# Performance work log

Hardware: AMD Instinct MI355X
Metric: run time of the kernel (lower is better)

Reference implementation:

```python
import jax, jax.numpy as jnp
import numpy as np

NUM_HEADS = 8


def setup_inputs() -> dict:
    key = jax.random.key(0)
    ks = jax.random.split(key, 6)
    B, S, H = 2, 4096, 512
    Q = jax.random.normal(ks[0], (B, S, H), dtype=jnp.float32)
    K = jax.random.normal(ks[1], (B, S, H), dtype=jnp.float32)
    V = jax.random.normal(ks[2], (B, S, H), dtype=jnp.float32)
    risk_sigma = jax.random.uniform(ks[3], (B, 1), dtype=jnp.float32) * 0.2
    risk_lambda = jnp.array([2.0], dtype=jnp.float32)
    W_out = jax.random.normal(ks[4], (H, H), dtype=jnp.float32) * (1.0 / np.sqrt(H))
    b_out = jnp.zeros((H,), dtype=jnp.float32)
    return {"Q": Q, "K": K, "V": V, "risk_sigma": risk_sigma,
            "risk_lambda": risk_lambda, "W_out": W_out, "b_out": b_out}


def reference(Q, K, V, risk_sigma, risk_lambda, W_out, b_out):
    B, S, H = Q.shape
    nh = NUM_HEADS
    hd = H // nh
    # split heads: [B, S, nh, hd]
    q = Q.reshape(B, S, nh, hd)
    k = K.reshape(B, S, nh, hd)
    v = V.reshape(B, S, nh, hd)
    scale = 1.0 / jnp.sqrt(jnp.asarray(hd, dtype=Q.dtype))
    # [B, nh, S, S]
    scores = jnp.einsum('bshd,bthd->bhst', q, k) * scale
    # distance-based risk penalty
    pos = jnp.arange(S, dtype=Q.dtype)
    norm_dist = jnp.abs(pos[None, :] - pos[:, None]) / S  # [S, S]
    dist_sq = norm_dist ** 2
    sigma_c = jnp.clip(risk_sigma, 0.001, 0.2)            # [B, 1]
    sigma_n = (sigma_c - 0.001) / (0.2 - 0.001)
    lam = (risk_lambda / 10.0).reshape(())                 # scalar
    risk_term = lam * sigma_n[:, :, None, None] * dist_sq[None, None]  # [B,1,S,S]
    attn = jax.nn.softmax(scores - risk_term, axis=-1)
    ctx = jnp.einsum('bhst,bthd->bshd', attn, v).reshape(B, S, H)
    return ctx @ W_out.T + b_out
```

## Files before the change

kernel.cpp:

```cpp
#include <hip/hip_runtime.h>
#include <hip/hip_bf16.h>


#define S_LEN 4096
#define NHEAD 8
#define HD 64
#define HTOT 512

typedef __attribute__((ext_vector_type(8))) short short8;
typedef __attribute__((ext_vector_type(4))) float floatx4;
typedef __attribute__((ext_vector_type(8))) _Float16 half8;

#if __has_builtin(__builtin_amdgcn_exp2f)
#define EXP2F(x) __builtin_amdgcn_exp2f(x)
#else
#define EXP2F(x) exp2f(x)
#endif

__device__ __forceinline__ unsigned pack_bf16(float a, float b) {
    unsigned ua = __builtin_bit_cast(unsigned, a) + 0x8000u;
    unsigned ub = __builtin_bit_cast(unsigned, b) + 0x8000u;
    return __builtin_amdgcn_perm(ub, ua, 0x07060302u);
}

__device__ __forceinline__ unsigned short f2bf(float x) {
    unsigned u = __builtin_bit_cast(unsigned, x) + 0x8000u;
    return (unsigned short)(u >> 16);
}

__device__ __forceinline__ void async16(const unsigned short* g, unsigned short* l) {
    __builtin_amdgcn_global_load_lds(
        (const __attribute__((address_space(1))) unsigned int*)g,
        (__attribute__((address_space(3))) unsigned int*)l, 16, 0, 0);
}

__global__ __launch_bounds__(256) void prep_kernel(
    const float* __restrict__ K, unsigned short* __restrict__ K16,
    const float* __restrict__ V, unsigned short* __restrict__ Vt)
{
    const int tid = threadIdx.x;
    if (blockIdx.x < 2048) {
        size_t i = ((size_t)blockIdx.x * 256 + tid) * 8;
        float4 a = *(const float4*)(K + i);
        float4 b = *(const float4*)(K + i + 4);
        unsigned o[4] = {pack_bf16(a.x, a.y), pack_bf16(a.z, a.w),
                         pack_bf16(b.x, b.y), pack_bf16(b.z, b.w)};
        *(short8*)(K16 + i) = *(short8*)o;
    } else {
        __shared__ unsigned short T[64 * 66];
        const int blk = blockIdx.x - 2048;
        const int st = blk & 63;
        const int bh = blk >> 6;
        const int b = bh >> 3, h = bh & 7;
        const float* src = V + ((size_t)b * S_LEN + st * 64) * HTOT + h * HD;
        for (int i = 0; i < 4; i++) {
            int idx = tid + i * 256;
            int s = idx >> 4, c4 = idx & 15;
            float4 v = *(const float4*)(src + (size_t)s * HTOT + c4 * 4);
            T[(c4 * 4 + 0) * 66 + s] = f2bf(v.x);
            T[(c4 * 4 + 1) * 66 + s] = f2bf(v.y);
            T[(c4 * 4 + 2) * 66 + s] = f2bf(v.z);
            T[(c4 * 4 + 3) * 66 + s] = f2bf(v.w);
        }
        __syncthreads();
        unsigned short* dst = Vt + ((size_t)bh * 64) * S_LEN + st * 64;
        for (int i = 0; i < 2; i++) {
            int idx = tid + i * 256;
            int d = idx >> 3, c8 = idx & 7;
            uint2 lo = *(const uint2*)&T[d * 66 + c8 * 8];
            uint2 hi = *(const uint2*)&T[d * 66 + c8 * 8 + 4];
            unsigned o[4] = {lo.x, lo.y, hi.x, hi.y};
            *(short8*)(dst + (size_t)d * S_LEN + c8 * 8) = *(short8*)o;
        }
    }
}

__global__ __launch_bounds__(256) void attn_kernel(
    const float* __restrict__ Q, const unsigned short* __restrict__ K16,
    const unsigned short* __restrict__ Vt,
    const float* __restrict__ risk_sigma, const float* __restrict__ risk_lambda,
    _Float16* __restrict__ Cpart, float* __restrict__ Lpart)
{
    __shared__ unsigned short QPsh[128 * 72];
    __shared__ unsigned short Ksh[2][64 * 64];
    __shared__ unsigned short Vsh[2][64 * 64];

    const int tid  = threadIdx.x;
    const int wave = tid >> 6;
    const int lane = tid & 63;
    const int quad = lane >> 4;
    const int ln   = lane & 15;
    const int sw   = ln & 7;

    const int bid = blockIdx.x;
    const int ks  = bid & 1;
    const int qt  = (bid >> 1) & 31;
    const int h   = (bid >> 6) & 7;
    const int b   = bid >> 9;
    const int qbase = qt * 128;

    float sig = risk_sigma[b];
    sig = fminf(fmaxf(sig, 0.001f), 0.2f);
    const float sn   = (sig - 0.001f) * (1.0f / 0.199f);
    const float coef = risk_lambda[0] * 0.1f * sn;
    const float nc2 = -coef * (1.0f / 4096.0f) * (1.0f / 4096.0f) * 1.4426950408889634f;
    const float qscale = 0.125f * 1.4426950408889634f;

    const float* Qb = Q + (size_t)b * S_LEN * HTOT + (size_t)h * HD;
    const unsigned short* Kb = K16 + (size_t)b * S_LEN * HTOT + (size_t)h * HD;
    const unsigned short* Vb = Vt + ((size_t)(b * 8 + h) * 64) * S_LEN;

    const int rl  = lane >> 3;
    const int c8g = ((lane & 7) ^ rl) << 3;
    auto dma = [&](int buf, int kbase) {
        const unsigned short* gk = Kb + (size_t)(kbase + wave * 8 + rl) * HTOT + c8g;
        const unsigned short* gv = Vb + (size_t)(wave * 8 + rl) * S_LEN + kbase + c8g;
        async16(gk,              &Ksh[buf][wave * 512 + lane * 8]);
        async16(gk + 32 * HTOT,  &Ksh[buf][(wave + 4) * 512 + lane * 8]);
        async16(gv,              &Vsh[buf][wave * 512 + lane * 8]);
        async16(gv + 32 * S_LEN, &Vsh[buf][(wave + 4) * 512 + lane * 8]);
    };

    dma(0, ks * 2048);
    for (int i = 0; i < 8; i++) {
        int idx = tid + i * 256;
        int r = idx >> 4, c4 = idx & 15;
        float4 v = *(const float4*)(Qb + (size_t)(qbase + r) * HTOT + c4 * 4);
        uint2 o;
        o.x = pack_bf16(v.x * qscale, v.y * qscale);
        o.y = pack_bf16(v.z * qscale, v.w * qscale);
        *(uint2*)&QPsh[r * 72 + c4 * 4] = o;
    }
    __syncthreads();

    short8 qf[2][2];
    for (int nt = 0; nt < 2; nt++) {
        qf[nt][0] = *(const short8*)&QPsh[(wave * 32 + nt * 16 + ln) * 72 + quad * 8];
        qf[nt][1] = *(const short8*)&QPsh[(wave * 32 + nt * 16 + ln) * 72 + 32 + quad * 8];
    }
    unsigned short* Pw = &QPsh[wave * 32 * 72];

    const short sone = (short)0x3F80;
    const short8 ones = {sone, sone, sone, sone, sone, sone, sone, sone};

    floatx4 Oacc[2][4], Lacc[2];
    for (int nt = 0; nt < 2; nt++) {
        Lacc[nt] = (floatx4){0.f, 0.f, 0.f, 0.f};
        for (int dt = 0; dt < 4; dt++) Oacc[nt][dt] = (floatx4){0.f, 0.f, 0.f, 0.f};
    }

    const int qa = qbase + wave * 32;

    for (int kt = 0; kt < 32; ++kt) {
        const int kbase = ks * 2048 + kt * 64;
        const int cur = kt & 1;
        if (kt < 31) dma(1 - cur, kbase + 64);
        const unsigned short* Kc = Ksh[cur];
        const unsigned short* Vc = Vsh[cur];

        const float dq = (float)(qa + ln - kbase);
        for (int jt = 0; jt < 4; jt++) {
            const int krow = (jt * 16 + ln) * 64;
            short8 ak0 = *(const short8*)&Kc[krow + ((quad ^ sw) << 3)];
            short8 ak1 = *(const short8*)&Kc[krow + (((quad + 4) ^ sw) << 3)];
            #pragma unroll
            for (int nt = 0; nt < 2; nt++) {
                floatx4 s = (floatx4){0.f, 0.f, 0.f, 0.f};
                s = __builtin_amdgcn_mfma_f32_16x16x32_bf16(ak0, qf[nt][0], s, 0, 0, 0);
                s = __builtin_amdgcn_mfma_f32_16x16x32_bf16(ak1, qf[nt][1], s, 0, 0, 0);
                float d = dq + (float)(nt * 16 - jt * 16 - quad * 4);
                float p[4];
                #pragma unroll
                for (int r = 0; r < 4; r++) {
                    float arg = __builtin_fmaf(nc2, d * d, s[r]);
                    p[r] = EXP2F(arg);
                    d -= 1.0f;
                }
                uint2 o;
                o.x = pack_bf16(p[0], p[1]);
                o.y = pack_bf16(p[2], p[3]);
                *(uint2*)&Pw[(nt * 16 + ln) * 72 + jt * 16 + quad * 4] = o;
            }
        }
        asm volatile("s_waitcnt lgkmcnt(0)" ::: "memory");
        __builtin_amdgcn_wave_barrier();

        short8 pf[2][2];
        for (int nt = 0; nt < 2; nt++) {
            pf[nt][0] = *(const short8*)&Pw[(nt * 16 + ln) * 72 + quad * 8];
            pf[nt][1] = *(const short8*)&Pw[(nt * 16 + ln) * 72 + 32 + quad * 8];
        }
        for (int dt = 0; dt < 4; dt++) {
            const int vrow = (dt * 16 + ln) * 64;
            short8 bv0 = *(const short8*)&Vc[vrow + ((quad ^ sw) << 3)];
            short8 bv1 = *(const short8*)&Vc[vrow + (((quad + 4) ^ sw) << 3)];
            #pragma unroll
            for (int nt = 0; nt < 2; nt++) {
                Oacc[nt][dt] = __builtin_amdgcn_mfma_f32_16x16x32_bf16(pf[nt][0], bv0, Oacc[nt][dt], 0, 0, 0);
                Oacc[nt][dt] = __builtin_amdgcn_mfma_f32_16x16x32_bf16(pf[nt][1], bv1, Oacc[nt][dt], 0, 0, 0);
            }
        }
        #pragma unroll
        for (int nt = 0; nt < 2; nt++) {
            Lacc[nt] = __builtin_amdgcn_mfma_f32_16x16x32_bf16(pf[nt][0], ones, Lacc[nt], 0, 0, 0);
            Lacc[nt] = __builtin_amdgcn_mfma_f32_16x16x32_bf16(pf[nt][1], ones, Lacc[nt], 0, 0, 0);
        }
        __syncthreads();
    }

    _Float16* Cw = Cpart + (size_t)bid * (128 * 64);
    for (int nt = 0; nt < 2; nt++) {
        if (ln == 0) {
            #pragma unroll
            for (int r = 0; r < 4; r++)
                Lpart[bid * 128 + wave * 32 + nt * 16 + quad * 4 + r] = Lacc[nt][r];
        }
        float rl4[4];
        #pragma unroll
        for (int r = 0; r < 4; r++) rl4[r] = 1.0f / Lacc[nt][r];
        for (int dt = 0; dt < 4; dt++)
            #pragma unroll
            for (int r = 0; r < 4; r++) {
                int q = wave * 32 + nt * 16 + quad * 4 + r;
                Cw[q * 64 + dt * 16 + ln] = (_Float16)(Oacc[nt][dt][r] * rl4[r]);
            }
    }
}

__global__ __launch_bounds__(256) void projc_kernel(
    const _Float16* __restrict__ Cpart, const float* __restrict__ Lpart,
    const float* __restrict__ W, const float* __restrict__ bias,
    float* __restrict__ out)
{
    __shared__ unsigned short Ash[64 * 40];
    __shared__ unsigned short Bsh[128 * 40];
    __shared__ float2 Lw[8][64];

    const int tid = threadIdx.x;
    const int wave = tid >> 6, lane = tid & 63, quad = lane >> 4, ln = lane & 15;
    const int wr = wave >> 1, wc = wave & 1;
    const int m0 = blockIdx.y * 64;
    const int nb = blockIdx.x * 128;
    const int b = m0 >> 12, qt = (m0 >> 7) & 31, qoff = m0 & 127;

    for (int i = 0; i < 2; i++) {
        int e = tid + i * 256;
        int hh = e >> 6, r = e & 63;
        int tile = (b * 8 + hh) * 32 + qt;
        float l0 = Lpart[(size_t)(tile * 2 + 0) * 128 + qoff + r];
        float l1 = Lpart[(size_t)(tile * 2 + 1) * 128 + qoff + r];
        float inv = 1.0f / (l0 + l1);
        Lw[hh][r] = (float2){l0 * inv, l1 * inv};
    }

    floatx4 acc[2][4];
    for (int i = 0; i < 2; i++)
        for (int j = 0; j < 4; j++) acc[i][j] = (floatx4){0.f, 0.f, 0.f, 0.f};

    const int ar = tid >> 2, ac8 = tid & 3;

    for (int kt = 0; kt < 16; ++kt) {
        const int k0 = kt * 32;
        const int h = k0 >> 6, d0 = k0 & 63;
        __syncthreads();
        {
            int tile = (b * 8 + h) * 32 + qt;
            const _Float16* C0 = Cpart + (size_t)(tile * 2) * (128 * 64)
                                 + (size_t)(qoff + ar) * 64 + d0 + ac8 * 8;
            const _Float16* C1 = C0 + 128 * 64;
            half8 a0 = *(const half8*)C0;
            half8 a1 = *(const half8*)C1;
            float2 w = Lw[h][ar];
            unsigned o[4];
            #pragma unroll
            for (int k = 0; k < 4; k++) {
                float v0 = w.x * (float)a0[2 * k]     + w.y * (float)a1[2 * k];
                float v1 = w.x * (float)a0[2 * k + 1] + w.y * (float)a1[2 * k + 1];
                o[k] = pack_bf16(v0, v1);
            }
            *(short8*)&Ash[ar * 40 + ac8 * 8] = *(short8*)o;
        }
        for (int i = 0; i < 4; i++) {
            int idx = tid + i * 256;
            int r = idx >> 3, c4 = idx & 7;
            float4 v = *(const float4*)&W[(size_t)(nb + r) * 512 + k0 + c4 * 4];
            uint2 o;
            o.x = pack_bf16(v.x, v.y);
            o.y = pack_bf16(v.z, v.w);
            *(uint2*)&Bsh[r * 40 + c4 * 4] = o;
        }
        __syncthreads();
        short8 af[2], bf[4];
        for (int i = 0; i < 2; i++)
            af[i] = *(const short8*)&Ash[(wr * 32 + i * 16 + ln) * 40 + quad * 8];
        for (int j = 0; j < 4; j++)
            bf[j] = *(const short8*)&Bsh[(wc * 64 + j * 16 + ln) * 40 + quad * 8];
        for (int i = 0; i < 2; i++)
            for (int j = 0; j < 4; j++)
                acc[i][j] = __builtin_amdgcn_mfma_f32_16x16x32_bf16(af[i], bf[j], acc[i][j], 0, 0, 0);
    }

    for (int i = 0; i < 2; i++) {
        int row = m0 + wr * 32 + i * 16 + quad * 4;
        for (int j = 0; j < 4; j++) {
            int col = nb + wc * 64 + j * 16 + ln;
            float bv = bias[col];
            #pragma unroll
            for (int r = 0; r < 4; r++)
                out[(size_t)(row + r) * 512 + col] = acc[i][j][r] + bv;
        }
    }
}

extern "C" void kernel_launch(void* const* d_in, const int* in_sizes, int n_in,
                              void* d_out, int out_size, void* d_ws, size_t ws_size,
                              hipStream_t stream) {
    const float* Q    = (const float*)d_in[0];
    const float* K    = (const float*)d_in[1];
    const float* V    = (const float*)d_in[2];
    const float* sig  = (const float*)d_in[3];
    const float* lam  = (const float*)d_in[4];
    const float* W    = (const float*)d_in[5];
    const float* bias = (const float*)d_in[6];

    unsigned short* K16 = (unsigned short*)d_ws;
    unsigned short* Vt  = (unsigned short*)((char*)d_ws + (8u << 20));
    _Float16* Cpart     = (_Float16*)((char*)d_ws + (16u << 20));
    float* Lpart        = (float*)((char*)d_ws + (32u << 20));
    float* out = (float*)d_out;

    prep_kernel<<<dim3(3072), dim3(256), 0, stream>>>(K, K16, V, Vt);
    attn_kernel<<<dim3(1024), dim3(256), 0, stream>>>(Q, K16, Vt, sig, lam, Cpart, Lpart);
    projc_kernel<<<dim3(4, 128), dim3(256), 0, stream>>>(Cpart, Lpart, W, bias, out);
}
```

Baseline: 233.8 us.

## Split combine from projection and double-buffer projection GEMM with async LDS loads

The fused combine-plus-projection kernel becomes two kernels. A combine kernel merges the two KV-split partial outputs into a bf16 context tensor. The projection kernel then double-buffers bf16 A and W tiles through global_load_lds with an XOR-swizzled layout, and W is pre-converted to bf16 in the prep kernel. This removes the per-iteration fp32-to-bf16 conversion and the redundant re-combine from the GEMM loop, at the cost of an extra launch and an extra round trip of the context tensor through memory. Cpart is now stored in the output buffer to save workspace.

New measurement: 228.9 us. -2.1%, faster.

```diff
diff --git a/kernel.cpp b/kernel.cpp
--- a/kernel.cpp
+++ b/kernel.cpp
@@ -10,6 +10,7 @@
 typedef __attribute__((ext_vector_type(8))) short short8;
 typedef __attribute__((ext_vector_type(4))) float floatx4;
 typedef __attribute__((ext_vector_type(8))) _Float16 half8;
+typedef __attribute__((ext_vector_type(2))) _Float16 half2v;
 
 #if __has_builtin(__builtin_amdgcn_exp2f)
 #define EXP2F(x) __builtin_amdgcn_exp2f(x)
@@ -36,10 +37,18 @@
 
 __global__ __launch_bounds__(256) void prep_kernel(
     const float* __restrict__ K, unsigned short* __restrict__ K16,
-    const float* __restrict__ V, unsigned short* __restrict__ Vt)
+    const float* __restrict__ V, unsigned short* __restrict__ Vt,
+    const float* __restrict__ W, unsigned short* __restrict__ W16)
 {
     const int tid = threadIdx.x;
-    if (blockIdx.x < 2048) {
+    if (blockIdx.x >= 3072) {
+        size_t i = ((size_t)(blockIdx.x - 3072) * 256 + tid) * 8;
+        float4 a = *(const float4*)(W + i);
+        float4 b = *(const float4*)(W + i + 4);
+        unsigned o[4] = {pack_bf16(a.x, a.y), pack_bf16(a.z, a.w),
+                         pack_bf16(b.x, b.y), pack_bf16(b.z, b.w)};
+        *(short8*)(W16 + i) = *(short8*)o;
+    } else if (blockIdx.x < 2048) {
         size_t i = ((size_t)blockIdx.x * 256 + tid) * 8;
         float4 a = *(const float4*)(K + i);
         float4 b = *(const float4*)(K + i + 4);
@@ -227,74 +236,94 @@
     }
 }
 
-__global__ __launch_bounds__(256) void projc_kernel(
+__global__ __launch_bounds__(256) void combine_kernel(
     const _Float16* __restrict__ Cpart, const float* __restrict__ Lpart,
-    const float* __restrict__ W, const float* __restrict__ bias,
+    unsigned short* __restrict__ ctx)
+{
+    const int t = threadIdx.x;
+    const int tile = blockIdx.x;
+    const int qt = tile & 31, h = (tile >> 5) & 7, b = tile >> 8;
+    __shared__ float w0s[128], w1s[128];
+    if (t < 128) {
+        float l0 = Lpart[(tile * 2 + 0) * 128 + t];
+        float l1 = Lpart[(tile * 2 + 1) * 128 + t];
+        float inv = 1.0f / (l0 + l1);
+        w0s[t] = l0 * inv;
+        w1s[t] = l1 * inv;
+    }
+    __syncthreads();
+    const _Float16* C0 = Cpart + (size_t)(tile * 2) * (128 * 64);
+    const _Float16* C1 = C0 + 128 * 64;
+    for (int i = 0; i < 8; i++) {
+        int e = (i * 256 + t) * 4;
+        int q = e >> 6, d = e & 63;
+        half2v a0 = *(const half2v*)(C0 + e);
+        half2v a1 = *(const half2v*)(C0 + e + 2);
+        half2v b0 = *(const half2v*)(C1 + e);
+        half2v b1 = *(const half2v*)(C1 + e + 2);
+        float w0 = w0s[q], w1 = w1s[q];
+        float v0 = w0 * (float)a0[0] + w1 * (float)b0[0];
+        float v1 = w0 * (float)a0[1] + w1 * (float)b0[1];
+        float v2 = w0 * (float)a1[0] + w1 * (float)b1[0];
+        float v3 = w0 * (float)a1[1] + w1 * (float)b1[1];
+        uint2 o;
+        o.x = pack_bf16(v0, v1);
+        o.y = pack_bf16(v2, v3);
+        *(uint2*)&ctx[((size_t)b * S_LEN + qt * 128 + q) * HTOT + h * HD + d] = o;
+    }
+}
+
+__global__ __launch_bounds__(256) void proj_kernel(
+    const unsigned short* __restrict__ A,
+    const unsigned short* __restrict__ W16,
+    const float* __restrict__ bias,
     float* __restrict__ out)
 {
-    __shared__ unsigned short Ash[64 * 40];
-    __shared__ unsigned short Bsh[128 * 40];
-    __shared__ float2 Lw[8][64];
-
+    __shared__ unsigned short Ash[2][64 * 32];
+    __shared__ unsigned short Bsh[2][128 * 32];
     const int tid = threadIdx.x;
     const int wave = tid >> 6, lane = tid & 63, quad = lane >> 4, ln = lane & 15;
     const int wr = wave >> 1, wc = wave & 1;
     const int m0 = blockIdx.y * 64;
     const int nb = blockIdx.x * 128;
-    const int b = m0 >> 12, qt = (m0 >> 7) & 31, qoff = m0 & 127;
-
-    for (int i = 0; i < 2; i++) {
-        int e = tid + i * 256;
-        int hh = e >> 6, r = e & 63;
-        int tile = (b * 8 + hh) * 32 + qt;
-        float l0 = Lpart[(size_t)(tile * 2 + 0) * 128 + qoff + r];
-        float l1 = Lpart[(size_t)(tile * 2 + 1) * 128 + qoff + r];
-        float inv = 1.0f / (l0 + l1);
-        Lw[hh][r] = (float2){l0 * inv, l1 * inv};
-    }
+
+    const int arow = (wave * 64 + lane) >> 2;
+    const int ac   = (wave * 64 + lane) & 3;
+    const int acs  = (ac ^ ((arow >> 1) & 3)) << 3;
+    const int wrow0 = (wave * 64 + lane) >> 2;
+    const int wc0   = (wave * 64 + lane) & 3;
+    const int wcs0  = (wc0 ^ ((wrow0 >> 1) & 3)) << 3;
+    const int wrow1 = wrow0 + 64;
+    const int wcs1  = (wc0 ^ ((wrow1 >> 1) & 3)) << 3;
+
+    auto dma = [&](int buf, int k0) {
+        async16(A + (size_t)(m0 + arow) * 512 + k0 + acs,
+                &Ash[buf][wave * 512 + lane * 8]);
+        async16(W16 + (size_t)(nb + wrow0) * 512 + k0 + wcs0,
+                &Bsh[buf][wave * 512 + lane * 8]);
+        async16(W16 + (size_t)(nb + wrow1) * 512 + k0 + wcs1,
+                &Bsh[buf][(wave + 4) * 512 + lane * 8]);
+    };
 
     floatx4 acc[2][4];
     for (int i = 0; i < 2; i++)
         for (int j = 0; j < 4; j++) acc[i][j] = (floatx4){0.f, 0.f, 0.f, 0.f};
 
-    const int ar = tid >> 2, ac8 = tid & 3;
-
+    dma(0, 0);
     for (int kt = 0; kt < 16; ++kt) {
-        const int k0 = kt * 32;
-        const int h = k0 >> 6, d0 = k0 & 63;
+        const int cur = kt & 1;
         __syncthreads();
-        {
-            int tile = (b * 8 + h) * 32 + qt;
-            const _Float16* C0 = Cpart + (size_t)(tile * 2) * (128 * 64)
-                                 + (size_t)(qoff + ar) * 64 + d0 + ac8 * 8;
-            const _Float16* C1 = C0 + 128 * 64;
-            half8 a0 = *(const half8*)C0;
-            half8 a1 = *(const half8*)C1;
-            float2 w = Lw[h][ar];
-            unsigned o[4];
-            #pragma unroll
-            for (int k = 0; k < 4; k++) {
-                float v0 = w.x * (float)a0[2 * k]     + w.y * (float)a1[2 * k];
-                float v1 = w.x * (float)a0[2 * k + 1] + w.y * (float)a1[2 * k + 1];
-                o[k] = pack_bf16(v0, v1);
-            }
-            *(short8*)&Ash[ar * 40 + ac8 * 8] = *(short8*)o;
-        }
-        for (int i = 0; i < 4; i++) {
-            int idx = tid + i * 256;
-            int r = idx >> 3, c4 = idx & 7;
-            float4 v = *(const float4*)&W[(size_t)(nb + r) * 512 + k0 + c4 * 4];
-            uint2 o;
-            o.x = pack_bf16(v.x, v.y);
-            o.y = pack_bf16(v.z, v.w);
-            *(uint2*)&Bsh[r * 40 + c4 * 4] = o;
-        }
-        __syncthreads();
+        if (kt < 15) dma(1 - cur, (kt + 1) * 32);
+
         short8 af[2], bf[4];
-        for (int i = 0; i < 2; i++)
-            af[i] = *(const short8*)&Ash[(wr * 32 + i * 16 + ln) * 40 + quad * 8];
-        for (int j = 0; j < 4; j++)
-            bf[j] = *(const short8*)&Bsh[(wc * 64 + j * 16 + ln) * 40 + quad * 8];
+        for (int i = 0; i < 2; i++) {
+            int r = wr * 32 + i * 16 + ln;
+            af[i] = *(const short8*)&Ash[cur][r * 32 + ((quad ^ ((r >> 1) & 3)) << 3)];
+        }
+        for (int j = 0; j < 4; j++) {
+            int r = wc * 64 + j * 16 + ln;
+            bf[j] = *(const short8*)&Bsh[cur][r * 32 + ((quad ^ ((r >> 1) & 3)) << 3)];
+        }
         for (int i = 0; i < 2; i++)
             for (int j = 0; j < 4; j++)
                 acc[i][j] = __builtin_amdgcn_mfma_f32_16x16x32_bf16(af[i], bf[j], acc[i][j], 0, 0, 0);
@@ -325,11 +354,14 @@
 
     unsigned short* K16 = (unsigned short*)d_ws;
     unsigned short* Vt  = (unsigned short*)((char*)d_ws + (8u << 20));
-    _Float16* Cpart     = (_Float16*)((char*)d_ws + (16u << 20));
-    float* Lpart        = (float*)((char*)d_ws + (32u << 20));
+    unsigned short* ctx = (unsigned short*)((char*)d_ws + (16u << 20));
+    float* Lpart        = (float*)((char*)d_ws + (24u << 20));
+    unsigned short* W16 = (unsigned short*)((char*)d_ws + (24u << 20) + (512u << 10));
+    _Float16* Cpart     = (_Float16*)d_out;
     float* out = (float*)d_out;
 
-    prep_kernel<<<dim3(3072), dim3(256), 0, stream>>>(K, K16, V, Vt);
+    prep_kernel<<<dim3(3200), dim3(256), 0, stream>>>(K, K16, V, Vt, W, W16);
     attn_kernel<<<dim3(1024), dim3(256), 0, stream>>>(Q, K16, Vt, sig, lam, Cpart, Lpart);
-    projc_kernel<<<dim3(4, 128), dim3(256), 0, stream>>>(Cpart, Lpart, W, bias, out);
-}
+    combine_kernel<<<dim3(512), dim3(256), 0, stream>>>(Cpart, Lpart, ctx);
+    proj_kernel<<<dim3(4, 128), dim3(256), 0, stream>>>(ctx, W16, bias, out);
+}
```
